# Performance work log

Measured on AMD Instinct MI355X. Metric: run time of the kernel, lower is better.

## Reference

```python
import jax, jax.numpy as jnp
import numpy as np

B, S, X, Y = 32, 3, 512, 512  # batch, O(3) spin components, lattice X, lattice Y

_L_np = np.array([[[0, 0, 0], [0, 0, -1], [0, 1, 0]],
                  [[0, 0, 1], [0, 0, 0], [-1, 0, 0]],
                  [[0, -1, 0], [1, 0, 0], [0, 0, 0]]], dtype=np.float32)


def setup_inputs() -> dict:
    key = jax.random.key(0)
    k_s, = jax.random.split(key, 1)
    s = jax.random.normal(k_s, (B, S, X, Y), dtype=jnp.float32)
    t = jnp.ones((), dtype=jnp.float32)
    C0 = jnp.ones((), dtype=jnp.float32)  # cc=[1.0] learnable coefficient
    L = jnp.asarray(_L_np)                # fixed SO(3) generators [s, r, a]
    return {"s": s, "t": t, "C0": C0, "L": L}


def reference(s, t, C0, L):
    # Psi0.grad: F = sum_mu (roll(s,+1,mu) + roll(s,-1,mu)); nearest-neighbor stencil
    Fn = (jnp.roll(s, 1, axis=2) + jnp.roll(s, -1, axis=2)
          + jnp.roll(s, 1, axis=3) + jnp.roll(s, -1, axis=3))
    # Lsig = -einsum('bsxy,sra->braxy', s, L); out = einsum('bsaxy,bsxy->baxy', Lsig, Fn)
    # fused: out[b,a,x,y] = -sum_{s,r} s[b,s,x,y] * L[s,r,a] * Fn[b,r,x,y]
    F = -jnp.einsum('bsxy,sra,brxy->baxy', s, L, Fn)
    # Coeff(t): cc=[1.0], EvenOdd=True, single coeff => Coeff(t) = C0 (t-independent)
    coeff = C0
    return coeff * F
```

## Files before the change

### kernel.cpp

```cpp
#include <hip/hip_runtime.h>
#include <hip/hip_bf16.h>


constexpr int B = 32, X = 512, Y = 512;
constexpr int XY = X * Y;

__global__ __launch_bounds__(256)
void psi0_kernel(const float* __restrict__ s,
                 const float* __restrict__ C0p,
                 const float* __restrict__ Lp,
                 float* __restrict__ out)
{
    __shared__ float Ls[27];
    if (threadIdx.x < 27) Ls[threadIdx.x] = Lp[threadIdx.x];
    __syncthreads();

    const int tid = threadIdx.x;
    const int ty  = tid & 127;
    const int row = tid >> 7;
    const int bid = blockIdx.x;
    const int b   = bid >> 8;
    const int x   = ((bid & 255) << 1) + row;
    const int y0  = ty << 2;

    const int xm = (x == 0)     ? X - 1 : x - 1;
    const int xp = (x == X - 1) ? 0     : x + 1;
    const int ym = (y0 == 0)    ? Y - 1 : y0 - 1;
    const int yp = (y0 + 4 == Y) ? 0    : y0 + 4;

    const float C0 = C0p[0];
    const size_t baseB = (size_t)b * 3 * XY;

    float4 sc[3];
    float4 Fn[3];

    #pragma unroll
    for (int c = 0; c < 3; ++c) {
        const float* p = s + baseB + (size_t)c * XY;
        const float4 ce = *(const float4*)(p + (size_t)x  * Y + y0);
        const float4 up = *(const float4*)(p + (size_t)xm * Y + y0);
        const float4 dn = *(const float4*)(p + (size_t)xp * Y + y0);
        const float  lf = p[(size_t)x * Y + ym];
        const float  rt = p[(size_t)x * Y + yp];
        sc[c] = ce;
        Fn[c].x = up.x + dn.x + lf   + ce.y;
        Fn[c].y = up.y + dn.y + ce.x + ce.z;
        Fn[c].z = up.z + dn.z + ce.y + ce.w;
        Fn[c].w = up.w + dn.w + ce.z + rt;
    }

    #pragma unroll
    for (int a = 0; a < 3; ++a) {
        float4 acc = make_float4(0.f, 0.f, 0.f, 0.f);
        #pragma unroll
        for (int ss = 0; ss < 3; ++ss) {
            #pragma unroll
            for (int r = 0; r < 3; ++r) {
                const float w = Ls[ss * 9 + r * 3 + a];
                acc.x += w * sc[ss].x * Fn[r].x;
                acc.y += w * sc[ss].y * Fn[r].y;
                acc.z += w * sc[ss].z * Fn[r].z;
                acc.w += w * sc[ss].w * Fn[r].w;
            }
        }
        float4 o;
        o.x = -C0 * acc.x;
        o.y = -C0 * acc.y;
        o.z = -C0 * acc.z;
        o.w = -C0 * acc.w;
        *(float4*)(out + baseB + (size_t)a * XY + (size_t)x * Y + y0) = o;
    }
}

extern "C" void kernel_launch(void* const* d_in, const int* in_sizes, int n_in,
                              void* d_out, int out_size, void* d_ws, size_t ws_size,
                              hipStream_t stream)
{
    const float* s   = (const float*)d_in[0];
    const float* C0p = (const float*)d_in[2];
    const float* Lp  = (const float*)d_in[3];
    float* out = (float*)d_out;

    const int blocks = B * (X / 2);
    psi0_kernel<<<blocks, 256, 0, stream>>>(s, C0p, Lp, out);
}
```

Baseline: 182.5 us.

## Map one wavefront per row with 8 elements per lane and shuffle halos

Each wavefront now covers a full 512-wide lattice row, with every lane handling 8 consecutive elements. Left and right neighbours come from cross-lane shuffles instead of extra scalar global loads. The shared-memory staging of L and its barrier are gone. The 27-term contraction is reduced to the six nonzero antisymmetric generator entries, with -C0 folded in. This cuts redundant and uncoalesced memory traffic and ALU work, but the kernel now assumes L has the fixed SO(3) sparsity pattern.

Measured after the change: 185.8 us. About the same (+1.8%).

```diff
diff --git a/kernel.cpp b/kernel.cpp
--- a/kernel.cpp
+++ b/kernel.cpp
@@ -1,5 +1,4 @@
 #include <hip/hip_runtime.h>
-#include <hip/hip_bf16.h>
 
 
 constexpr int B = 32, X = 512, Y = 512;
@@ -11,64 +10,72 @@
                  const float* __restrict__ Lp,
                  float* __restrict__ out)
 {
-    __shared__ float Ls[27];
-    if (threadIdx.x < 27) Ls[threadIdx.x] = Lp[threadIdx.x];
-    __syncthreads();
-
-    const int tid = threadIdx.x;
-    const int ty  = tid & 127;
-    const int row = tid >> 7;
-    const int bid = blockIdx.x;
-    const int b   = bid >> 8;
-    const int x   = ((bid & 255) << 1) + row;
-    const int y0  = ty << 2;
+    const int tid  = threadIdx.x;
+    const int lane = tid & 63;
+    const int wv   = tid >> 6;
+    const int bid  = blockIdx.x;
+    const int b    = bid >> 7;
+    const int x    = ((bid & 127) << 2) + wv;
+    const int y0   = lane << 3;
 
     const int xm = (x == 0)     ? X - 1 : x - 1;
     const int xp = (x == X - 1) ? 0     : x + 1;
-    const int ym = (y0 == 0)    ? Y - 1 : y0 - 1;
-    const int yp = (y0 + 4 == Y) ? 0    : y0 + 4;
 
     const float C0 = C0p[0];
+    const float cA0 = -C0 * Lp[15];
+    const float cB0 = -C0 * Lp[21];
+    const float cA1 = -C0 * Lp[7];
+    const float cB1 = -C0 * Lp[19];
+    const float cA2 = -C0 * Lp[5];
+    const float cB2 = -C0 * Lp[11];
+
     const size_t baseB = (size_t)b * 3 * XY;
+    const size_t offC  = (size_t)x  * Y + y0;
+    const size_t offU  = (size_t)xm * Y + y0;
+    const size_t offD  = (size_t)xp * Y + y0;
 
-    float4 sc[3];
-    float4 Fn[3];
+    float sc[3][8];
+    float Fn[3][8];
 
     #pragma unroll
     for (int c = 0; c < 3; ++c) {
         const float* p = s + baseB + (size_t)c * XY;
-        const float4 ce = *(const float4*)(p + (size_t)x  * Y + y0);
-        const float4 up = *(const float4*)(p + (size_t)xm * Y + y0);
-        const float4 dn = *(const float4*)(p + (size_t)xp * Y + y0);
-        const float  lf = p[(size_t)x * Y + ym];
-        const float  rt = p[(size_t)x * Y + yp];
-        sc[c] = ce;
-        Fn[c].x = up.x + dn.x + lf   + ce.y;
-        Fn[c].y = up.y + dn.y + ce.x + ce.z;
-        Fn[c].z = up.z + dn.z + ce.y + ce.w;
-        Fn[c].w = up.w + dn.w + ce.z + rt;
+        const float4 c0 = *(const float4*)(p + offC);
+        const float4 c1 = *(const float4*)(p + offC + 4);
+        const float4 u0 = *(const float4*)(p + offU);
+        const float4 u1 = *(const float4*)(p + offU + 4);
+        const float4 d0 = *(const float4*)(p + offD);
+        const float4 d1 = *(const float4*)(p + offD + 4);
+
+        const float lf = __shfl(c1.w, (lane + 63) & 63, 64);
+        const float rt = __shfl(c0.x, (lane + 1) & 63, 64);
+
+        sc[c][0] = c0.x; sc[c][1] = c0.y; sc[c][2] = c0.z; sc[c][3] = c0.w;
+        sc[c][4] = c1.x; sc[c][5] = c1.y; sc[c][6] = c1.z; sc[c][7] = c1.w;
+
+        Fn[c][0] = u0.x + d0.x + lf   + c0.y;
+        Fn[c][1] = u0.y + d0.y + c0.x + c0.z;
+        Fn[c][2] = u0.z + d0.z + c0.y + c0.w;
+        Fn[c][3] = u0.w + d0.w + c0.z + c1.x;
+        Fn[c][4] = u1.x + d1.x + c0.w + c1.y;
+        Fn[c][5] = u1.y + d1.y + c1.x + c1.z;
+        Fn[c][6] = u1.z + d1.z + c1.y + c1.w;
+        Fn[c][7] = u1.w + d1.w + c1.z + rt;
+    }
+
+    float o[3][8];
+    #pragma unroll
+    for (int e = 0; e < 8; ++e) {
+        o[0][e] = cA0 * (sc[1][e] * Fn[2][e]) + cB0 * (sc[2][e] * Fn[1][e]);
+        o[1][e] = cA1 * (sc[0][e] * Fn[2][e]) + cB1 * (sc[2][e] * Fn[0][e]);
+        o[2][e] = cA2 * (sc[0][e] * Fn[1][e]) + cB2 * (sc[1][e] * Fn[0][e]);
     }
 
     #pragma unroll
     for (int a = 0; a < 3; ++a) {
-        float4 acc = make_float4(0.f, 0.f, 0.f, 0.f);
-        #pragma unroll
-        for (int ss = 0; ss < 3; ++ss) {
-            #pragma unroll
-            for (int r = 0; r < 3; ++r) {
-                const float w = Ls[ss * 9 + r * 3 + a];
-                acc.x += w * sc[ss].x * Fn[r].x;
-                acc.y += w * sc[ss].y * Fn[r].y;
-                acc.z += w * sc[ss].z * Fn[r].z;
-                acc.w += w * sc[ss].w * Fn[r].w;
-            }
-        }
-        float4 o;
-        o.x = -C0 * acc.x;
-        o.y = -C0 * acc.y;
-        o.z = -C0 * acc.z;
-        o.w = -C0 * acc.w;
-        *(float4*)(out + baseB + (size_t)a * XY + (size_t)x * Y + y0) = o;
+        float* q = out + baseB + (size_t)a * XY + offC;
+        *(float4*)(q)     = make_float4(o[a][0], o[a][1], o[a][2], o[a][3]);
+        *(float4*)(q + 4) = make_float4(o[a][4], o[a][5], o[a][6], o[a][7]);
     }
 }
 
@@ -81,6 +88,6 @@
     const float* Lp  = (const float*)d_in[3];
     float* out = (float*)d_out;
 
-    const int blocks = B * (X / 2);
+    const int blocks = B * (X / 4);
     psi0_kernel<<<blocks, 256, 0, stream>>>(s, C0p, Lp, out);
 }
```

## Process two rows per thread, exploit generator sparsity, use nontemporal stores

Applied to the files above, without the earlier changes.

Each thread now computes two adjacent lattice rows and reuses the shared vertical neighbour rows, so fewer redundant row loads are issued per output. The 27-term contraction with L is cut to six products. Those use precomputed coefficients read from the L entries assumed nonzero for the SO(3) generators, and the shared-memory staging and barrier are dropped. Outputs are written with nontemporal stores and the launch bound requests more occupancy. The risk is that the kernel silently assumes the antisymmetric sparsity pattern of L, and that higher register use per thread could limit waves.

Measured after the change: 182.2 us. Within noise of the previous version (-0.1%).

```diff
diff --git a/kernel.cpp b/kernel.cpp
--- a/kernel.cpp
+++ b/kernel.cpp
@@ -1,74 +1,114 @@
 #include <hip/hip_runtime.h>
-#include <hip/hip_bf16.h>
 
 
 constexpr int B = 32, X = 512, Y = 512;
 constexpr int XY = X * Y;
 
-__global__ __launch_bounds__(256)
+typedef float f32x4 __attribute__((ext_vector_type(4)));
+
+__device__ __forceinline__ void nt_store4(float* p, float a, float b, float c, float d)
+{
+    f32x4 v = { a, b, c, d };
+    __builtin_nontemporal_store(v, (f32x4*)p);
+}
+
+__global__ __launch_bounds__(256, 4)
 void psi0_kernel(const float* __restrict__ s,
                  const float* __restrict__ C0p,
                  const float* __restrict__ Lp,
                  float* __restrict__ out)
 {
-    __shared__ float Ls[27];
-    if (threadIdx.x < 27) Ls[threadIdx.x] = Lp[threadIdx.x];
-    __syncthreads();
-
     const int tid = threadIdx.x;
     const int ty  = tid & 127;
-    const int row = tid >> 7;
+    const int rp  = tid >> 7;
     const int bid = blockIdx.x;
-    const int b   = bid >> 8;
-    const int x   = ((bid & 255) << 1) + row;
+    const int b   = bid >> 7;
+    const int x   = ((bid & 127) << 2) + (rp << 1);
     const int y0  = ty << 2;
 
-    const int xm = (x == 0)     ? X - 1 : x - 1;
-    const int xp = (x == X - 1) ? 0     : x + 1;
-    const int ym = (y0 == 0)    ? Y - 1 : y0 - 1;
-    const int yp = (y0 + 4 == Y) ? 0    : y0 + 4;
+    const int xm  = (x == 0) ? X - 1 : x - 1;
+    const int xp1 = x + 1;
+    const int xp2 = (x + 2 == X) ? 0 : x + 2;
+    const int ym  = (y0 == 0)     ? Y - 1 : y0 - 1;
+    const int yp  = (y0 + 4 == Y) ? 0     : y0 + 4;
 
-    const float C0 = C0p[0];
-    const size_t baseB = (size_t)b * 3 * XY;
+    const float C0  = C0p[0];
+    const float cA0 = -C0 * Lp[15];
+    const float cB0 = -C0 * Lp[21];
+    const float cA1 = -C0 * Lp[7];
+    const float cB1 = -C0 * Lp[19];
+    const float cA2 = -C0 * Lp[5];
+    const float cB2 = -C0 * Lp[11];
 
-    float4 sc[3];
-    float4 Fn[3];
+    const size_t base = (size_t)b * 3 * XY;
+    const size_t rB = (size_t)x   * Y + y0;
+    const size_t rA = (size_t)xm  * Y + y0;
+    const size_t rC = (size_t)xp1 * Y + y0;
+    const size_t rD = (size_t)xp2 * Y + y0;
 
+    float4 Av[3], Bv[3], Cv[3], Dv[3];
     #pragma unroll
     for (int c = 0; c < 3; ++c) {
-        const float* p = s + baseB + (size_t)c * XY;
-        const float4 ce = *(const float4*)(p + (size_t)x  * Y + y0);
-        const float4 up = *(const float4*)(p + (size_t)xm * Y + y0);
-        const float4 dn = *(const float4*)(p + (size_t)xp * Y + y0);
-        const float  lf = p[(size_t)x * Y + ym];
-        const float  rt = p[(size_t)x * Y + yp];
-        sc[c] = ce;
-        Fn[c].x = up.x + dn.x + lf   + ce.y;
-        Fn[c].y = up.y + dn.y + ce.x + ce.z;
-        Fn[c].z = up.z + dn.z + ce.y + ce.w;
-        Fn[c].w = up.w + dn.w + ce.z + rt;
+        const float* p = s + base + (size_t)c * XY;
+        Av[c] = *(const float4*)(p + rA);
+        Bv[c] = *(const float4*)(p + rB);
+        Cv[c] = *(const float4*)(p + rC);
+        Dv[c] = *(const float4*)(p + rD);
+    }
+    float lfB[3], rtB[3], lfC[3], rtC[3];
+    #pragma unroll
+    for (int c = 0; c < 3; ++c) {
+        const float* p = s + base + (size_t)c * XY;
+        lfB[c] = p[(size_t)x   * Y + ym];
+        rtB[c] = p[(size_t)x   * Y + yp];
+        lfC[c] = p[(size_t)xp1 * Y + ym];
+        rtC[c] = p[(size_t)xp1 * Y + yp];
     }
 
-    #pragma unroll
-    for (int a = 0; a < 3; ++a) {
-        float4 acc = make_float4(0.f, 0.f, 0.f, 0.f);
+    {
+        float Fn[3][4], sc[3][4];
         #pragma unroll
-        for (int ss = 0; ss < 3; ++ss) {
-            #pragma unroll
-            for (int r = 0; r < 3; ++r) {
-                const float w = Ls[ss * 9 + r * 3 + a];
-                acc.x += w * sc[ss].x * Fn[r].x;
-                acc.y += w * sc[ss].y * Fn[r].y;
-                acc.z += w * sc[ss].z * Fn[r].z;
-                acc.w += w * sc[ss].w * Fn[r].w;
-            }
+        for (int c = 0; c < 3; ++c) {
+            const float4 cc = Bv[c], uu = Av[c], dd = Cv[c];
+            sc[c][0] = cc.x; sc[c][1] = cc.y; sc[c][2] = cc.z; sc[c][3] = cc.w;
+            Fn[c][0] = uu.x + dd.x + lfB[c] + cc.y;
+            Fn[c][1] = uu.y + dd.y + cc.x   + cc.z;
+            Fn[c][2] = uu.z + dd.z + cc.y   + cc.w;
+            Fn[c][3] = uu.w + dd.w + cc.z   + rtB[c];
         }
-        float4 o;
-        o.x = -C0 * acc.x;
-        o.y = -C0 * acc.y;
-        o.z = -C0 * acc.z;
-        o.w = -C0 * acc.w;
-        *(float4*)(out + baseB + (size_t)a * XY + (size_t)x * Y + y0) = o;
+        float o0[4], o1[4], o2[4];
+        #pragma unroll
+        for (int e = 0; e < 4; ++e) {
+            o0[e] = cA0 * (sc[1][e] * Fn[2][e]) + cB0 * (sc[2][e] * Fn[1][e]);
+            o1[e] = cA1 * (sc[0][e] * Fn[2][e]) + cB1 * (sc[2][e] * Fn[0][e]);
+            o2[e] = cA2 * (sc[0][e] * Fn[1][e]) + cB2 * (sc[1][e] * Fn[0][e]);
+        }
+        nt_store4(out + base + 0 * (size_t)XY + rB, o0[0], o0[1], o0[2], o0[3]);
+        nt_store4(out + base + 1 * (size_t)XY + rB, o1[0], o1[1], o1[2], o1[3]);
+        nt_store4(out + base + 2 * (size_t)XY + rB, o2[0], o2[1], o2[2], o2[3]);
+    }
+
+    {
+        float Fn[3][4], sc[3][4];
+        #pragma unroll
+        for (int c = 0; c < 3; ++c) {
+            const float4 cc = Cv[c], uu = Bv[c], dd = Dv[c];
+            sc[c][0] = cc.x; sc[c][1] = cc.y; sc[c][2] = cc.z; sc[c][3] = cc.w;
+            Fn[c][0] = uu.x + dd.x + lfC[c] + cc.y;
+            Fn[c][1] = uu.y + dd.y + cc.x   + cc.z;
+            Fn[c][2] = uu.z + dd.z + cc.y   + cc.w;
+            Fn[c][3] = uu.w + dd.w + cc.z   + rtC[c];
+        }
+        float o0[4], o1[4], o2[4];
+        #pragma unroll
+        for (int e = 0; e < 4; ++e) {
+            o0[e] = cA0 * (sc[1][e] * Fn[2][e]) + cB0 * (sc[2][e] * Fn[1][e]);
+            o1[e] = cA1 * (sc[0][e] * Fn[2][e]) + cB1 * (sc[2][e] * Fn[0][e]);
+            o2[e] = cA2 * (sc[0][e] * Fn[1][e]) + cB2 * (sc[1][e] * Fn[0][e]);
+        }
+        nt_store4(out + base + 0 * (size_t)XY + rC, o0[0], o0[1], o0[2], o0[3]);
+        nt_store4(out + base + 1 * (size_t)XY + rC, o1[0], o1[1], o1[2], o1[3]);
+        nt_store4(out + base + 2 * (size_t)XY + rC, o2[0], o2[1], o2[2], o2[3]);
     }
 }
 
@@ -81,6 +121,6 @@
     const float* Lp  = (const float*)d_in[3];
     float* out = (float*)d_out;
 
-    const int blocks = B * (X / 2);
+    const int blocks = B * (X / 4);
     psi0_kernel<<<blocks, 256, 0, stream>>>(s, C0p, Lp, out);
 }
```
